# Optimization experiments

Hardware: AMD Instinct MI355X
Metric: run time of the kernel (lower is better)

## Reference

```python
import jax, jax.numpy as jnp
from jax import lax
import numpy as np

IN_F, H1, OUT_F, P = 128, 64, 64, 0.25
B, T = 64, 2048


def setup_inputs() -> dict:
    key = jax.random.key(0)
    ks = jax.random.split(key, 12)
    def w(k, shape, fan_in):
        return jax.random.normal(k, shape, dtype=jnp.float32) / np.sqrt(fan_in).astype(np.float32)
    x = jax.random.normal(ks[0], (B, T, IN_F), dtype=jnp.float32)
    # PyTorch LSTM param layout: W_ih [4H, in], W_hh [4H, H], gate order i,f,g,o
    W_ih1 = w(ks[1], (4 * H1, IN_F), IN_F)
    W_hh1 = w(ks[2], (4 * H1, H1), H1)
    b_ih1 = jnp.zeros((4 * H1,), jnp.float32)
    b_hh1 = jnp.zeros((4 * H1,), jnp.float32)
    W_ih2 = w(ks[3], (4 * OUT_F, H1), H1)
    W_hh2 = w(ks[4], (4 * OUT_F, OUT_F), OUT_F)
    b_ih2 = jnp.zeros((4 * OUT_F,), jnp.float32)
    b_hh2 = jnp.zeros((4 * OUT_F,), jnp.float32)
    # Variational (locked) dropout masks: one per sequence, shared across timesteps,
    # inverted-dropout pre-scaled by 1/(1-p).
    keep = 1.0 - P
    mask1 = (jax.random.bernoulli(ks[5], keep, (B, H1)).astype(jnp.float32) / keep)
    mask2 = (jax.random.bernoulli(ks[6], keep, (B, OUT_F)).astype(jnp.float32) / keep)
    return {"x": x, "W_ih1": W_ih1, "W_hh1": W_hh1, "b_ih1": b_ih1, "b_hh1": b_hh1,
            "W_ih2": W_ih2, "W_hh2": W_hh2, "b_ih2": b_ih2, "b_hh2": b_hh2,
            "mask1": mask1, "mask2": mask2}


def _lstm(x, W_ih, W_hh, b_ih, b_hh):
    # x: [B,T,I]; returns all hidden states [B,T,H]
    Bd = x.shape[0]
    H = W_hh.shape[1]
    # Precompute input contribution for all timesteps (one big GEMM).
    xg = jnp.einsum('bti,gi->btg', x, W_ih) + b_ih + b_hh  # [B,T,4H]
    W_hh_T = W_hh.T  # [H,4H]
    def step(carry, xg_t):
        h, c = carry
        g = xg_t + h @ W_hh_T
        i, f, gg, o = jnp.split(g, 4, axis=-1)
        c = jax.nn.sigmoid(f) * c + jax.nn.sigmoid(i) * jnp.tanh(gg)
        h = jax.nn.sigmoid(o) * jnp.tanh(c)
        return (h, c), h
    h0 = jnp.zeros((Bd, H), x.dtype)
    c0 = jnp.zeros((Bd, H), x.dtype)
    _, hs = lax.scan(step, (h0, c0), jnp.swapaxes(xg, 0, 1))
    return jnp.swapaxes(hs, 0, 1)


def reference(x, W_ih1, W_hh1, b_ih1, b_hh1, W_ih2, W_hh2, b_ih2, b_hh2, mask1, mask2):
    out = _lstm(x, W_ih1, W_hh1, b_ih1, b_hh1) * mask1[:, None, :]
    out = _lstm(out, W_ih2, W_hh2, b_ih2, b_hh2) * mask2[:, None, :]
    return jax.nn.relu(out)
```

## Files before the change

### kernel.cpp

```cpp
#include <hip/hip_runtime.h>
#include <hip/hip_bf16.h>

#define BB 64
#define TT 2048
#define INF 128
#define HH 64
#define GG 256

__device__ __forceinline__ float sigm(float x) { return 1.0f / (1.0f + __expf(-x)); }
__device__ __forceinline__ float tanh_f(float x) {
  float e = __expf(2.0f * x);
  return 1.0f - 2.0f / (e + 1.0f);
}
__device__ __forceinline__ float bcast(float v, int l) {
  return __uint_as_float(__builtin_amdgcn_readlane(__float_as_uint(v), l));
}


#define XWL1(I)                                                   \
  { float4 a = Wp[t * 32 + (I)];                                  \
    w0[4*(I)] = a.x; w0[4*(I)+1] = a.y; w0[4*(I)+2] = a.z; w0[4*(I)+3] = a.w; \
    float4 b = Wp[(128 + t) * 32 + (I)];                          \
    w1[4*(I)] = b.x; w1[4*(I)+1] = b.y; w1[4*(I)+2] = b.z; w1[4*(I)+3] = b.w; }
#define XWL4(I) XWL1(I) XWL1((I)+1) XWL1((I)+2) XWL1((I)+3)
#define XWLOAD XWL4(0) XWL4(4) XWL4(8) XWL4(12) XWL4(16) XWL4(20) XWL4(24) XWL4(28)

#define XD1(L)                                                    \
  { float xa = bcast(curx, (L)); float xb = bcast(cury, (L));     \
    a0e = fmaf(xa, w0[2*(L)],   a0e); a0o = fmaf(xb, w0[2*(L)+1], a0o); \
    a1e = fmaf(xa, w1[2*(L)],   a1e); a1o = fmaf(xb, w1[2*(L)+1], a1o); }
#define XD8(L) XD1(L) XD1((L)+1) XD1((L)+2) XD1((L)+3) XD1((L)+4) XD1((L)+5) XD1((L)+6) XD1((L)+7)
#define XDOT64 XD8(0) XD8(8) XD8(16) XD8(24) XD8(32) XD8(40) XD8(48) XD8(56)

__global__ __launch_bounds__(128, 1) void xgemm(const float* __restrict__ X,
                                                const float* __restrict__ W,
                                                const float* __restrict__ bi,
                                                const float* __restrict__ bh,
                                                float* __restrict__ XG) {
  const int t = threadIdx.x;
  const int lane = t & 63;
  const long m0 = (long)blockIdx.x * 256;

  float w0[INF], w1[INF];
  const float4* Wp = (const float4*)W;
  XWLOAD
  const float bias0 = bi[t] + bh[t];
  const float bias1 = bi[128 + t] + bh[128 + t];

  const float2* Xp = (const float2*)X;
  float2 cur = Xp[(size_t)m0 * 64 + lane];
  float2 nx1 = Xp[(size_t)(m0 + 1) * 64 + lane];

  for (int mi = 0; mi < 256; ++mi) {
    const long m = m0 + mi;
    float2 nx2 = make_float2(0.f, 0.f);
    if (mi + 2 < 256) nx2 = Xp[(size_t)(m + 2) * 64 + lane];

    const float curx = cur.x, cury = cur.y;
    float a0e = bias0, a0o = 0.f, a1e = bias1, a1o = 0.f;
    XDOT64
    XG[(size_t)m * GG + t] = a0e + a0o;
    XG[(size_t)m * GG + 128 + t] = a1e + a1o;
    cur = nx1; nx1 = nx2;
  }
}

#define WL1(I)                                                                  \
  { float4 a = p[lane * 16 + (I)];                                              \
    wi[4*(I)] = a.x; wi[4*(I)+1] = a.y; wi[4*(I)+2] = a.z; wi[4*(I)+3] = a.w;   \
    float4 c = p[(64 + lane) * 16 + (I)];                                       \
    wf[4*(I)] = c.x; wf[4*(I)+1] = c.y; wf[4*(I)+2] = c.z; wf[4*(I)+3] = c.w;   \
    float4 d = p[(128 + lane) * 16 + (I)];                                      \
    wg[4*(I)] = d.x; wg[4*(I)+1] = d.y; wg[4*(I)+2] = d.z; wg[4*(I)+3] = d.w;   \
    float4 e = p[(192 + lane) * 16 + (I)];                                      \
    wo[4*(I)] = e.x; wo[4*(I)+1] = e.y; wo[4*(I)+2] = e.z; wo[4*(I)+3] = e.w; }
#define WL4(I) WL1(I) WL1((I)+1) WL1((I)+2) WL1((I)+3)
#define WLOAD WL4(0) WL4(4) WL4(8) WL4(12)

#define D1(K)                                              \
  { float hk = bcast(hv, (K));                             \
    ai = fmaf(hk, wi[(K)], ai); af = fmaf(hk, wf[(K)], af);\
    ag = fmaf(hk, wg[(K)], ag); ao = fmaf(hk, wo[(K)], ao); }
#define D8(K) D1(K) D1((K)+1) D1((K)+2) D1((K)+3) D1((K)+4) D1((K)+5) D1((K)+6) D1((K)+7)
#define DOT64 D8(0) D8(8) D8(16) D8(24) D8(32) D8(40) D8(48) D8(56)

__global__ __launch_bounds__(256, 1) void lstm2(const float* __restrict__ XG,
                                                const float* __restrict__ Whh1,
                                                const float* __restrict__ Wih2,
                                                const float* __restrict__ Whh2,
                                                const float* __restrict__ bi2,
                                                const float* __restrict__ bh2,
                                                const float* __restrict__ m1g,
                                                const float* __restrict__ m2g,
                                                float* __restrict__ out) {
  const int b = blockIdx.x;
  const int wid = threadIdx.x >> 6;
  const int lane = threadIdx.x & 63;

  __shared__ int f_w0, f_w1, f_w2;
  __shared__ __align__(16) float x2buf[4][HH];
  __shared__ __align__(16) float a2xbuf[4][GG];

  if (threadIdx.x == 0) { f_w0 = 0; f_w1 = 0; f_w2 = 0; }
  __syncthreads();
  if (wid == 3) return;

#define WAIT_GE(flag, tgt)                                   \
  do {                                                       \
    while (*(volatile int*)&(flag) < (tgt)) {}               \
    asm volatile("" ::: "memory");                           \
  } while (0)
#define PUBLISH(flag, val)                                   \
  do {                                                       \
    asm volatile("s_waitcnt lgkmcnt(0)" ::: "memory");       \
    if (lane == 0) *(volatile int*)&(flag) = (val);          \
  } while (0)

  if (wid == 0) {
    float wi[HH], wf[HH], wg[HH], wo[HH];
    const float4* p = (const float4*)Whh1;
    WLOAD
    const float m1 = m1g[b * HH + lane];
    const float* xgp = XG + (size_t)b * TT * GG;

    float cur0 = xgp[lane], cur1 = xgp[64 + lane], cur2 = xgp[128 + lane], cur3 = xgp[192 + lane];
    float n10 = xgp[GG + lane], n11 = xgp[GG + 64 + lane], n12 = xgp[GG + 128 + lane], n13 = xgp[GG + 192 + lane];

    float h1 = 0.f, c1 = 0.f;
    for (int s = 0; s < TT; ++s) {
      float n20 = 0.f, n21 = 0.f, n22 = 0.f, n23 = 0.f;
      if (s + 2 < TT) {
        const float* q = xgp + (size_t)(s + 2) * GG;
        n20 = q[lane]; n21 = q[64 + lane]; n22 = q[128 + lane]; n23 = q[192 + lane];
      }

      const float hv = h1;
      float ai = cur0, af = cur1, ag = cur2, ao = cur3;
      DOT64
      c1 = sigm(af) * c1 + sigm(ai) * tanh_f(ag);
      h1 = sigm(ao) * tanh_f(c1);

      WAIT_GE(f_w1, s - 3);
      x2buf[s & 3][lane] = h1 * m1;
      PUBLISH(f_w0, s + 1);

      cur0 = n10; cur1 = n11; cur2 = n12; cur3 = n13;
      n10 = n20; n11 = n21; n12 = n22; n13 = n23;
    }
  } else if (wid == 1) {
    float wi[HH], wf[HH], wg[HH], wo[HH];
    const float4* p = (const float4*)Wih2;
    WLOAD
    const float bi_i = bi2[lane] + bh2[lane];
    const float bi_f = bi2[64 + lane] + bh2[64 + lane];
    const float bi_g = bi2[128 + lane] + bh2[128 + lane];
    const float bi_o = bi2[192 + lane] + bh2[192 + lane];

    for (int s = 0; s < TT; ++s) {
      WAIT_GE(f_w0, s + 1);
      const float hv = x2buf[s & 3][lane];

      float ai = bi_i, af = bi_f, ag = bi_g, ao = bi_o;
      DOT64
      WAIT_GE(f_w2, s - 3);
      a2xbuf[s & 3][lane] = ai;
      a2xbuf[s & 3][64 + lane] = af;
      a2xbuf[s & 3][128 + lane] = ag;
      a2xbuf[s & 3][192 + lane] = ao;
      PUBLISH(f_w1, s + 1);
    }
  } else {
    float wi[HH], wf[HH], wg[HH], wo[HH];
    const float4* p = (const float4*)Whh2;
    WLOAD
    const float m2 = m2g[b * HH + lane];
    float* ob = out + (size_t)b * TT * HH;

    float h2 = 0.f, c2 = 0.f;
    for (int s = 0; s < TT; ++s) {
      const float hv = h2;
      float ai = 0.f, af = 0.f, ag = 0.f, ao = 0.f;
      DOT64

      WAIT_GE(f_w1, s + 1);
      ai += a2xbuf[s & 3][lane];
      af += a2xbuf[s & 3][64 + lane];
      ag += a2xbuf[s & 3][128 + lane];
      ao += a2xbuf[s & 3][192 + lane];

      c2 = sigm(af) * c2 + sigm(ai) * tanh_f(ag);
      h2 = sigm(ao) * tanh_f(c2);
      PUBLISH(f_w2, s + 1);
      ob[(size_t)s * HH + lane] = fmaxf(h2 * m2, 0.f);
    }
  }
#undef WAIT_GE
#undef PUBLISH
}

extern "C" void kernel_launch(void* const* d_in, const int* in_sizes, int n_in,
                              void* d_out, int out_size, void* d_ws, size_t ws_size,
                              hipStream_t stream) {
  (void)in_sizes; (void)n_in; (void)out_size; (void)ws_size;
  const float* x     = (const float*)d_in[0];
  const float* W_ih1 = (const float*)d_in[1];
  const float* W_hh1 = (const float*)d_in[2];
  const float* b_ih1 = (const float*)d_in[3];
  const float* b_hh1 = (const float*)d_in[4];
  const float* W_ih2 = (const float*)d_in[5];
  const float* W_hh2 = (const float*)d_in[6];
  const float* b_ih2 = (const float*)d_in[7];
  const float* b_hh2 = (const float*)d_in[8];
  const float* mask1 = (const float*)d_in[9];
  const float* mask2 = (const float*)d_in[10];
  float* out = (float*)d_out;

  float* xg1 = (float*)d_ws;

  xgemm<<<dim3(BB * TT / 256), dim3(128), 0, stream>>>(x, W_ih1, b_ih1, b_hh1, xg1);
  lstm2<<<dim3(BB), dim3(256), 0, stream>>>(xg1, W_hh1, W_ih2, W_hh2, b_ih2, b_hh2,
                                            mask1, mask2, out);
}
```

Measured before the change: 2.522 ms.

## Split layer-2 input projection across two waves and deepen LSTM pipeline ring buffers

The previously idle fourth wave now takes the odd timesteps of the layer-2 input projection, so two waves (even/odd) feed the layer-2 recurrence through separate flags. The ring buffers grow from 4 to 8 slots, layer 1 processes two timesteps per publish, flag polls are cached locally to skip redundant LDS reads, and layer 2 speculatively loads its input when it is already available. The xgemm grid also doubles with half the rows per block. The aim is to take the projection wave off the critical path of the serial recurrence, at the cost of more complex synchronization.

Result: slower. 3.867 ms (+53.3%).

```diff
diff --git a/kernel.cpp b/kernel.cpp
--- a/kernel.cpp
+++ b/kernel.cpp
@@ -39,7 +39,7 @@
                                                 float* __restrict__ XG) {
   const int t = threadIdx.x;
   const int lane = t & 63;
-  const long m0 = (long)blockIdx.x * 256;
+  const long m0 = (long)blockIdx.x * 128;
 
   float w0[INF], w1[INF];
   const float4* Wp = (const float4*)W;
@@ -51,10 +51,10 @@
   float2 cur = Xp[(size_t)m0 * 64 + lane];
   float2 nx1 = Xp[(size_t)(m0 + 1) * 64 + lane];
 
-  for (int mi = 0; mi < 256; ++mi) {
+  for (int mi = 0; mi < 128; ++mi) {
     const long m = m0 + mi;
     float2 nx2 = make_float2(0.f, 0.f);
-    if (mi + 2 < 256) nx2 = Xp[(size_t)(m + 2) * 64 + lane];
+    if (mi + 2 < 128) nx2 = Xp[(size_t)(m + 2) * 64 + lane];
 
     const float curx = cur.x, cury = cur.y;
     float a0e = bias0, a0o = 0.f, a1e = bias1, a1o = 0.f;
@@ -97,23 +97,29 @@
   const int wid = threadIdx.x >> 6;
   const int lane = threadIdx.x & 63;
 
-  __shared__ int f_w0, f_w1, f_w2;
-  __shared__ __align__(16) float x2buf[4][HH];
-  __shared__ __align__(16) float a2xbuf[4][GG];
-
-  if (threadIdx.x == 0) { f_w0 = 0; f_w1 = 0; f_w2 = 0; }
+  __shared__ int f_w0, f_e, f_o, f_w2;
+  __shared__ __align__(16) float x2buf[8][HH];
+  __shared__ __align__(16) float a2xbuf[8][GG];
+
+  if (threadIdx.x == 0) { f_w0 = 0; f_e = 0; f_o = 0; f_w2 = 0; }
   __syncthreads();
-  if (wid == 3) return;
-
-#define WAIT_GE(flag, tgt)                                   \
-  do {                                                       \
-    while (*(volatile int*)&(flag) < (tgt)) {}               \
-    asm volatile("" ::: "memory");                           \
+
+#define WAITC(seen, flag, tgt)                                  \
+  do {                                                          \
+    if ((seen) < (tgt)) {                                       \
+      while (((seen) = *(volatile int*)&(flag)) < (tgt)) {}     \
+    }                                                           \
+    asm volatile("" ::: "memory");                              \
   } while (0)
-#define PUBLISH(flag, val)                                   \
-  do {                                                       \
-    asm volatile("s_waitcnt lgkmcnt(0)" ::: "memory");       \
-    if (lane == 0) *(volatile int*)&(flag) = (val);          \
+#define PUBLISH(flag, val)                                      \
+  do {                                                          \
+    asm volatile("s_waitcnt lgkmcnt(0)" ::: "memory");          \
+    if (lane == 0) *(volatile int*)&(flag) = (val);             \
+  } while (0)
+#define PUBLISHP(pflag, val)                                    \
+  do {                                                          \
+    asm volatile("s_waitcnt lgkmcnt(0)" ::: "memory");          \
+    if (lane == 0) *(pflag) = (val);                            \
   } while (0)
 
   if (wid == 0) {
@@ -123,31 +129,87 @@
     const float m1 = m1g[b * HH + lane];
     const float* xgp = XG + (size_t)b * TT * GG;
 
-    float cur0 = xgp[lane], cur1 = xgp[64 + lane], cur2 = xgp[128 + lane], cur3 = xgp[192 + lane];
-    float n10 = xgp[GG + lane], n11 = xgp[GG + 64 + lane], n12 = xgp[GG + 128 + lane], n13 = xgp[GG + 192 + lane];
+    float a0 = xgp[lane], a1 = xgp[64 + lane], a2 = xgp[128 + lane], a3 = xgp[192 + lane];
+    float b0 = xgp[GG + lane], b1 = xgp[GG + 64 + lane], b2 = xgp[GG + 128 + lane], b3 = xgp[GG + 192 + lane];
 
     float h1 = 0.f, c1 = 0.f;
-    for (int s = 0; s < TT; ++s) {
-      float n20 = 0.f, n21 = 0.f, n22 = 0.f, n23 = 0.f;
+    int seen_e = 0, seen_o = 0;
+    for (int s = 0; s < TT; s += 2) {
+      float p0 = 0.f, p1 = 0.f, p2 = 0.f, p3 = 0.f;
+      float q0 = 0.f, q1 = 0.f, q2 = 0.f, q3 = 0.f;
       if (s + 2 < TT) {
         const float* q = xgp + (size_t)(s + 2) * GG;
-        n20 = q[lane]; n21 = q[64 + lane]; n22 = q[128 + lane]; n23 = q[192 + lane];
-      }
-
-      const float hv = h1;
-      float ai = cur0, af = cur1, ag = cur2, ao = cur3;
+        p0 = q[lane]; p1 = q[64 + lane]; p2 = q[128 + lane]; p3 = q[192 + lane];
+        const float* r = q + GG;
+        q0 = r[lane]; q1 = r[64 + lane]; q2 = r[128 + lane]; q3 = r[192 + lane];
+      }
+
+      WAITC(seen_e, f_e, s - 7);
+      WAITC(seen_o, f_o, s - 6);
+
+      {
+        const float hv = h1;
+        float ai = a0, af = a1, ag = a2, ao = a3;
+        DOT64
+        c1 = sigm(af) * c1 + sigm(ai) * tanh_f(ag);
+        h1 = sigm(ao) * tanh_f(c1);
+        x2buf[s & 7][lane] = h1 * m1;
+      }
+      {
+        const float hv = h1;
+        float ai = b0, af = b1, ag = b2, ao = b3;
+        DOT64
+        c1 = sigm(af) * c1 + sigm(ai) * tanh_f(ag);
+        h1 = sigm(ao) * tanh_f(c1);
+        x2buf[(s + 1) & 7][lane] = h1 * m1;
+      }
+      PUBLISH(f_w0, s + 2);
+
+      a0 = p0; a1 = p1; a2 = p2; a3 = p3;
+      b0 = q0; b1 = q1; b2 = q2; b3 = q3;
+    }
+  } else if (wid == 2) {
+    float wi[HH], wf[HH], wg[HH], wo[HH];
+    const float4* p = (const float4*)Whh2;
+    WLOAD
+    const float m2 = m2g[b * HH + lane];
+    float* ob = out + (size_t)b * TT * HH;
+
+    float h2 = 0.f, c2 = 0.f;
+    int seen_e = 0, seen_o = 0;
+    for (int s = 0; s < TT; ++s) {
+      const int odd = s & 1;
+      const bool pre = odd ? (seen_o >= s + 1) : (seen_e >= s + 1);
+      float xi, xf, xg, xo;
+      if (pre) {
+        asm volatile("" ::: "memory");
+        xi = a2xbuf[s & 7][lane];
+        xf = a2xbuf[s & 7][64 + lane];
+        xg = a2xbuf[s & 7][128 + lane];
+        xo = a2xbuf[s & 7][192 + lane];
+      }
+
+      const float hv = h2;
+      float ai = 0.f, af = 0.f, ag = 0.f, ao = 0.f;
       DOT64
-      c1 = sigm(af) * c1 + sigm(ai) * tanh_f(ag);
-      h1 = sigm(ao) * tanh_f(c1);
-
-      WAIT_GE(f_w1, s - 3);
-      x2buf[s & 3][lane] = h1 * m1;
-      PUBLISH(f_w0, s + 1);
-
-      cur0 = n10; cur1 = n11; cur2 = n12; cur3 = n13;
-      n10 = n20; n11 = n21; n12 = n22; n13 = n23;
+
+      if (!pre) {
+        if (odd) { WAITC(seen_o, f_o, s + 1); }
+        else     { WAITC(seen_e, f_e, s + 1); }
+        xi = a2xbuf[s & 7][lane];
+        xf = a2xbuf[s & 7][64 + lane];
+        xg = a2xbuf[s & 7][128 + lane];
+        xo = a2xbuf[s & 7][192 + lane];
+      }
+      ai += xi; af += xf; ag += xg; ao += xo;
+
+      PUBLISH(f_w2, s + 1);
+
+      c2 = sigm(af) * c2 + sigm(ai) * tanh_f(ag);
+      h2 = sigm(ao) * tanh_f(c2);
+      ob[(size_t)s * HH + lane] = fmaxf(h2 * m2, 0.f);
     }
-  } else if (wid == 1) {
+  } else {
     float wi[HH], wf[HH], wg[HH], wo[HH];
     const float4* p = (const float4*)Wih2;
     WLOAD
@@ -156,46 +218,27 @@
     const float bi_g = bi2[128 + lane] + bh2[128 + lane];
     const float bi_o = bi2[192 + lane] + bh2[192 + lane];
 
-    for (int s = 0; s < TT; ++s) {
-      WAIT_GE(f_w0, s + 1);
-      const float hv = x2buf[s & 3][lane];
+    const int par = (wid == 3);
+    volatile int* const myflag = par ? &f_o : &f_e;
+    int seen0 = 0, seen2 = 0;
+    for (int s = par; s < TT; s += 2) {
+      WAITC(seen0, f_w0, s + 1);
+      const float hv = x2buf[s & 7][lane];
 
       float ai = bi_i, af = bi_f, ag = bi_g, ao = bi_o;
       DOT64
-      WAIT_GE(f_w2, s - 3);
-      a2xbuf[s & 3][lane] = ai;
-      a2xbuf[s & 3][64 + lane] = af;
-      a2xbuf[s & 3][128 + lane] = ag;
-      a2xbuf[s & 3][192 + lane] = ao;
-      PUBLISH(f_w1, s + 1);
-    }
-  } else {
-    float wi[HH], wf[HH], wg[HH], wo[HH];
-    const float4* p = (const float4*)Whh2;
-    WLOAD
-    const float m2 = m2g[b * HH + lane];
-    float* ob = out + (size_t)b * TT * HH;
-
-    float h2 = 0.f, c2 = 0.f;
-    for (int s = 0; s < TT; ++s) {
-      const float hv = h2;
-      float ai = 0.f, af = 0.f, ag = 0.f, ao = 0.f;
-      DOT64
-
-      WAIT_GE(f_w1, s + 1);
-      ai += a2xbuf[s & 3][lane];
-      af += a2xbuf[s & 3][64 + lane];
-      ag += a2xbuf[s & 3][128 + lane];
-      ao += a2xbuf[s & 3][192 + lane];
-
-      c2 = sigm(af) * c2 + sigm(ai) * tanh_f(ag);
-      h2 = sigm(ao) * tanh_f(c2);
-      PUBLISH(f_w2, s + 1);
-      ob[(size_t)s * HH + lane] = fmaxf(h2 * m2, 0.f);
+
+      WAITC(seen2, f_w2, s - 7);
+      a2xbuf[s & 7][lane] = ai;
+      a2xbuf[s & 7][64 + lane] = af;
+      a2xbuf[s & 7][128 + lane] = ag;
+      a2xbuf[s & 7][192 + lane] = ao;
+      PUBLISHP(myflag, s + 1);
     }
   }
-#undef WAIT_GE
+#undef WAITC
 #undef PUBLISH
+#undef PUBLISHP
 }
 
 extern "C" void kernel_launch(void* const* d_in, const int* in_sizes, int n_in,
@@ -217,7 +260,7 @@
 
   float* xg1 = (float*)d_ws;
 
-  xgemm<<<dim3(BB * TT / 256), dim3(128), 0, stream>>>(x, W_ih1, b_ih1, b_hh1, xg1);
+  xgemm<<<dim3(BB * TT / 128), dim3(128), 0, stream>>>(x, W_ih1, b_ih1, b_hh1, xg1);
   lstm2<<<dim3(BB), dim3(256), 0, stream>>>(xg1, W_hh1, W_ih2, W_hh2, b_ih2, b_hh2,
                                             mask1, mask2, out);
 }
```

## Split each LSTM recurrence across two wavefronts exchanging gate activations via LDS

Applied to the files above, without the earlier changes.

Each recurrent stage (layer-1 W_hh, layer-2 input projection, layer-2 W_hh) now runs on two wavefronts, each computing two of the four gates. The partner activations are exchanged through double-buffered LDS with flag handshakes, and both halves redundantly keep c and h. This halves the serial per-step FMA chain on the critical path, at the cost of an extra intra-block sync per step. Inter-stage buffers are deepened to 8 slots with cached flag reads, and the xgemm kernel now uses 256 threads with one gate row per thread.

Measured after the change: 2.729 ms. 1.08x slower.

```diff
diff --git a/kernel.cpp b/kernel.cpp
--- a/kernel.cpp
+++ b/kernel.cpp
@@ -15,24 +15,39 @@
 __device__ __forceinline__ float bcast(float v, int l) {
   return __uint_as_float(__builtin_amdgcn_readlane(__float_as_uint(v), l));
 }
-
-
-#define XWL1(I)                                                   \
-  { float4 a = Wp[t * 32 + (I)];                                  \
-    w0[4*(I)] = a.x; w0[4*(I)+1] = a.y; w0[4*(I)+2] = a.z; w0[4*(I)+3] = a.w; \
-    float4 b = Wp[(128 + t) * 32 + (I)];                          \
-    w1[4*(I)] = b.x; w1[4*(I)+1] = b.y; w1[4*(I)+2] = b.z; w1[4*(I)+3] = b.w; }
-#define XWL4(I) XWL1(I) XWL1((I)+1) XWL1((I)+2) XWL1((I)+3)
-#define XWLOAD XWL4(0) XWL4(4) XWL4(8) XWL4(12) XWL4(16) XWL4(20) XWL4(24) XWL4(28)
-
-#define XD1(L)                                                    \
-  { float xa = bcast(curx, (L)); float xb = bcast(cury, (L));     \
-    a0e = fmaf(xa, w0[2*(L)],   a0e); a0o = fmaf(xb, w0[2*(L)+1], a0o); \
-    a1e = fmaf(xa, w1[2*(L)],   a1e); a1o = fmaf(xb, w1[2*(L)+1], a1o); }
-#define XD8(L) XD1(L) XD1((L)+1) XD1((L)+2) XD1((L)+3) XD1((L)+4) XD1((L)+5) XD1((L)+6) XD1((L)+7)
-#define XDOT64 XD8(0) XD8(8) XD8(16) XD8(24) XD8(32) XD8(40) XD8(48) XD8(56)
-
-__global__ __launch_bounds__(128, 1) void xgemm(const float* __restrict__ X,
+__device__ __forceinline__ void lstm_upd(float Si, float Sf, float Tg, float So,
+                                         float& c, float& h) {
+  c = fmaf(Sf, c, Si * Tg);
+  h = So * tanh_f(c);
+}
+
+
+#define WL2(I)                                                                   \
+  { float4 a_ = p[lane * 16 + (I)];                                              \
+    wA[4*(I)] = a_.x; wA[4*(I)+1] = a_.y; wA[4*(I)+2] = a_.z; wA[4*(I)+3] = a_.w;\
+    float4 b_ = p[(64 + lane) * 16 + (I)];                                       \
+    wB[4*(I)] = b_.x; wB[4*(I)+1] = b_.y; wB[4*(I)+2] = b_.z; wB[4*(I)+3] = b_.w; }
+#define WL2x4(I) WL2(I) WL2((I)+1) WL2((I)+2) WL2((I)+3)
+#define WLOAD2 WL2x4(0) WL2x4(4) WL2x4(8) WL2x4(12)
+
+#define G1(K)                                                    \
+  { float hk = bcast(hv, (K));                                   \
+    aA = fmaf(hk, wA[(K)], aA); aB = fmaf(hk, wB[(K)], aB); }
+#define G8(K) G1(K) G1((K)+1) G1((K)+2) G1((K)+3) G1((K)+4) G1((K)+5) G1((K)+6) G1((K)+7)
+#define DOT2G G8(0) G8(8) G8(16) G8(24) G8(32) G8(40) G8(48) G8(56)
+
+#define YW1(I) { float4 a_ = Wp[t * 32 + (I)];                                   \
+    wr[4*(I)] = a_.x; wr[4*(I)+1] = a_.y; wr[4*(I)+2] = a_.z; wr[4*(I)+3] = a_.w; }
+#define YW4(I) YW1(I) YW1((I)+1) YW1((I)+2) YW1((I)+3)
+#define YWLOAD YW4(0) YW4(4) YW4(8) YW4(12) YW4(16) YW4(20) YW4(24) YW4(28)
+
+#define YD1(L)                                                   \
+  { float xa = bcast(curx, (L)); float xb = bcast(cury, (L));    \
+    ae = fmaf(xa, wr[2*(L)], ae); ao = fmaf(xb, wr[2*(L)+1], ao); }
+#define YD8(L) YD1(L) YD1((L)+1) YD1((L)+2) YD1((L)+3) YD1((L)+4) YD1((L)+5) YD1((L)+6) YD1((L)+7)
+#define YDOT64 YD8(0) YD8(8) YD8(16) YD8(24) YD8(32) YD8(40) YD8(48) YD8(56)
+
+__global__ __launch_bounds__(256, 1) void xgemm(const float* __restrict__ X,
                                                 const float* __restrict__ W,
                                                 const float* __restrict__ bi,
                                                 const float* __restrict__ bh,
@@ -41,11 +56,10 @@
   const int lane = t & 63;
   const long m0 = (long)blockIdx.x * 256;
 
-  float w0[INF], w1[INF];
+  float wr[INF];
   const float4* Wp = (const float4*)W;
-  XWLOAD
-  const float bias0 = bi[t] + bh[t];
-  const float bias1 = bi[128 + t] + bh[128 + t];
+  YWLOAD
+  const float bias = bi[t] + bh[t];
 
   const float2* Xp = (const float2*)X;
   float2 cur = Xp[(size_t)m0 * 64 + lane];
@@ -57,34 +71,14 @@
     if (mi + 2 < 256) nx2 = Xp[(size_t)(m + 2) * 64 + lane];
 
     const float curx = cur.x, cury = cur.y;
-    float a0e = bias0, a0o = 0.f, a1e = bias1, a1o = 0.f;
-    XDOT64
-    XG[(size_t)m * GG + t] = a0e + a0o;
-    XG[(size_t)m * GG + 128 + t] = a1e + a1o;
+    float ae = bias, ao = 0.f;
+    YDOT64
+    XG[(size_t)m * GG + t] = ae + ao;
     cur = nx1; nx1 = nx2;
   }
 }
 
-#define WL1(I)                                                                  \
-  { float4 a = p[lane * 16 + (I)];                                              \
-    wi[4*(I)] = a.x; wi[4*(I)+1] = a.y; wi[4*(I)+2] = a.z; wi[4*(I)+3] = a.w;   \
-    float4 c = p[(64 + lane) * 16 + (I)];                                       \
-    wf[4*(I)] = c.x; wf[4*(I)+1] = c.y; wf[4*(I)+2] = c.z; wf[4*(I)+3] = c.w;   \
-    float4 d = p[(128 + lane) * 16 + (I)];                                      \
-    wg[4*(I)] = d.x; wg[4*(I)+1] = d.y; wg[4*(I)+2] = d.z; wg[4*(I)+3] = d.w;   \
-    float4 e = p[(192 + lane) * 16 + (I)];                                      \
-    wo[4*(I)] = e.x; wo[4*(I)+1] = e.y; wo[4*(I)+2] = e.z; wo[4*(I)+3] = e.w; }
-#define WL4(I) WL1(I) WL1((I)+1) WL1((I)+2) WL1((I)+3)
-#define WLOAD WL4(0) WL4(4) WL4(8) WL4(12)
-
-#define D1(K)                                              \
-  { float hk = bcast(hv, (K));                             \
-    ai = fmaf(hk, wi[(K)], ai); af = fmaf(hk, wf[(K)], af);\
-    ag = fmaf(hk, wg[(K)], ag); ao = fmaf(hk, wo[(K)], ao); }
-#define D8(K) D1(K) D1((K)+1) D1((K)+2) D1((K)+3) D1((K)+4) D1((K)+5) D1((K)+6) D1((K)+7)
-#define DOT64 D8(0) D8(8) D8(16) D8(24) D8(32) D8(40) D8(48) D8(56)
-
-__global__ __launch_bounds__(256, 1) void lstm2(const float* __restrict__ XG,
+__global__ __launch_bounds__(384, 1) void lstm2(const float* __restrict__ XG,
                                                 const float* __restrict__ Whh1,
                                                 const float* __restrict__ Wih2,
                                                 const float* __restrict__ Whh2,
@@ -97,104 +91,173 @@
   const int wid = threadIdx.x >> 6;
   const int lane = threadIdx.x & 63;
 
-  __shared__ int f_w0, f_w1, f_w2;
-  __shared__ __align__(16) float x2buf[4][HH];
-  __shared__ __align__(16) float a2xbuf[4][GG];
-
-  if (threadIdx.x == 0) { f_w0 = 0; f_w1 = 0; f_w2 = 0; }
+  __shared__ int f_0A, f_0B, f_h1, f_xA, f_xB, f_2A, f_2B;
+  __shared__ __align__(16) float ex0A[2][2 * HH];
+  __shared__ __align__(16) float ex0B[2][2 * HH];
+  __shared__ __align__(16) float ex2A[2][2 * HH];
+  __shared__ __align__(16) float ex2B[2][2 * HH];
+  __shared__ __align__(16) float x2buf[8][HH];
+  __shared__ __align__(16) float a2xA[8][2 * HH];
+  __shared__ __align__(16) float a2xB[8][2 * HH];
+
+  if (threadIdx.x == 0) { f_0A = 0; f_0B = 0; f_h1 = 0; f_xA = 0; f_xB = 0; f_2A = 0; f_2B = 0; }
   __syncthreads();
-  if (wid == 3) return;
-
-#define WAIT_GE(flag, tgt)                                   \
-  do {                                                       \
-    while (*(volatile int*)&(flag) < (tgt)) {}               \
-    asm volatile("" ::: "memory");                           \
+
+#define WAITC(seen, flag, tgt)                                  \
+  do {                                                          \
+    if ((seen) < (tgt)) {                                       \
+      while (((seen) = *(volatile int*)&(flag)) < (tgt)) {}     \
+    }                                                           \
+    asm volatile("" ::: "memory");                              \
   } while (0)
-#define PUBLISH(flag, val)                                   \
-  do {                                                       \
-    asm volatile("s_waitcnt lgkmcnt(0)" ::: "memory");       \
-    if (lane == 0) *(volatile int*)&(flag) = (val);          \
+#define PUBLISH(flag, val)                                      \
+  do {                                                          \
+    asm volatile("s_waitcnt lgkmcnt(0)" ::: "memory");          \
+    if (lane == 0) *(volatile int*)&(flag) = (val);             \
   } while (0)
 
-  if (wid == 0) {
-    float wi[HH], wf[HH], wg[HH], wo[HH];
+  if (wid == 2) {
+    float wA[HH], wB[HH];
     const float4* p = (const float4*)Whh1;
-    WLOAD
+    WLOAD2
     const float m1 = m1g[b * HH + lane];
     const float* xgp = XG + (size_t)b * TT * GG;
 
-    float cur0 = xgp[lane], cur1 = xgp[64 + lane], cur2 = xgp[128 + lane], cur3 = xgp[192 + lane];
-    float n10 = xgp[GG + lane], n11 = xgp[GG + 64 + lane], n12 = xgp[GG + 128 + lane], n13 = xgp[GG + 192 + lane];
+    float xi0 = xgp[lane],      xf0 = xgp[64 + lane];
+    float xi1 = xgp[GG + lane], xf1 = xgp[GG + 64 + lane];
 
     float h1 = 0.f, c1 = 0.f;
-    for (int s = 0; s < TT; ++s) {
-      float n20 = 0.f, n21 = 0.f, n22 = 0.f, n23 = 0.f;
+    int s0B = 0, sxa = 0, sxb = 0;
+    for (int s = 0; s < TT; ++s) {
+      float xi2 = 0.f, xf2 = 0.f;
       if (s + 2 < TT) {
         const float* q = xgp + (size_t)(s + 2) * GG;
-        n20 = q[lane]; n21 = q[64 + lane]; n22 = q[128 + lane]; n23 = q[192 + lane];
+        xi2 = q[lane]; xf2 = q[64 + lane];
       }
-
       const float hv = h1;
-      float ai = cur0, af = cur1, ag = cur2, ao = cur3;
-      DOT64
-      c1 = sigm(af) * c1 + sigm(ai) * tanh_f(ag);
-      h1 = sigm(ao) * tanh_f(c1);
-
-      WAIT_GE(f_w1, s - 3);
-      x2buf[s & 3][lane] = h1 * m1;
-      PUBLISH(f_w0, s + 1);
-
-      cur0 = n10; cur1 = n11; cur2 = n12; cur3 = n13;
-      n10 = n20; n11 = n21; n12 = n22; n13 = n23;
-    }
-  } else if (wid == 1) {
-    float wi[HH], wf[HH], wg[HH], wo[HH];
+      float aA = xi0, aB = xf0;
+      DOT2G
+      const float Si = sigm(aA), Sf = sigm(aB);
+      ex0A[s & 1][lane] = Si; ex0A[s & 1][64 + lane] = Sf;
+      PUBLISH(f_0A, s + 1);
+      WAITC(s0B, f_0B, s + 1);
+      const float Tg = ex0B[s & 1][lane], So = ex0B[s & 1][64 + lane];
+      lstm_upd(Si, Sf, Tg, So, c1, h1);
+      WAITC(sxa, f_xA, s - 7);
+      WAITC(sxb, f_xB, s - 7);
+      x2buf[s & 7][lane] = h1 * m1;
+      PUBLISH(f_h1, s + 1);
+      xi0 = xi1; xf0 = xf1; xi1 = xi2; xf1 = xf2;
+    }
+  } else if (wid == 0) {
+    float wA[HH], wB[HH];
+    const float4* p = (const float4*)(Whh1 + 128 * HH);
+    WLOAD2
+    const float* xgp = XG + (size_t)b * TT * GG;
+
+    float xg0 = xgp[128 + lane],      xo0 = xgp[192 + lane];
+    float xg1 = xgp[GG + 128 + lane], xo1 = xgp[GG + 192 + lane];
+
+    float h1 = 0.f, c1 = 0.f;
+    int s0A = 0;
+    for (int s = 0; s < TT; ++s) {
+      float xg2 = 0.f, xo2 = 0.f;
+      if (s + 2 < TT) {
+        const float* q = xgp + (size_t)(s + 2) * GG;
+        xg2 = q[128 + lane]; xo2 = q[192 + lane];
+      }
+      const float hv = h1;
+      float aA = xg0, aB = xo0;
+      DOT2G
+      const float Tg = tanh_f(aA), So = sigm(aB);
+      ex0B[s & 1][lane] = Tg; ex0B[s & 1][64 + lane] = So;
+      PUBLISH(f_0B, s + 1);
+      WAITC(s0A, f_0A, s + 1);
+      const float Si = ex0A[s & 1][lane], Sf = ex0A[s & 1][64 + lane];
+      lstm_upd(Si, Sf, Tg, So, c1, h1);
+      xg0 = xg1; xo0 = xo1; xg1 = xg2; xo1 = xo2;
+    }
+  } else if (wid == 4) {
+    float wA[HH], wB[HH];
     const float4* p = (const float4*)Wih2;
-    WLOAD
-    const float bi_i = bi2[lane] + bh2[lane];
-    const float bi_f = bi2[64 + lane] + bh2[64 + lane];
-    const float bi_g = bi2[128 + lane] + bh2[128 + lane];
-    const float bi_o = bi2[192 + lane] + bh2[192 + lane];
-
-    for (int s = 0; s < TT; ++s) {
-      WAIT_GE(f_w0, s + 1);
-      const float hv = x2buf[s & 3][lane];
-
-      float ai = bi_i, af = bi_f, ag = bi_g, ao = bi_o;
-      DOT64
-      WAIT_GE(f_w2, s - 3);
-      a2xbuf[s & 3][lane] = ai;
-      a2xbuf[s & 3][64 + lane] = af;
-      a2xbuf[s & 3][128 + lane] = ag;
-      a2xbuf[s & 3][192 + lane] = ao;
-      PUBLISH(f_w1, s + 1);
+    WLOAD2
+    const float biA = bi2[lane] + bh2[lane];
+    const float biB = bi2[64 + lane] + bh2[64 + lane];
+
+    int sh = 0, sc = 0;
+    for (int s = 0; s < TT; ++s) {
+      WAITC(sh, f_h1, s + 1);
+      const float hv = x2buf[s & 7][lane];
+      float aA = biA, aB = biB;
+      DOT2G
+      WAITC(sc, f_2A, s - 7);
+      a2xA[s & 7][lane] = aA; a2xA[s & 7][64 + lane] = aB;
+      PUBLISH(f_xA, s + 1);
+    }
+  } else if (wid == 5) {
+    float wA[HH], wB[HH];
+    const float4* p = (const float4*)(Wih2 + 128 * HH);
+    WLOAD2
+    const float biA = bi2[128 + lane] + bh2[128 + lane];
+    const float biB = bi2[192 + lane] + bh2[192 + lane];
+
+    int sh = 0, sc = 0;
+    for (int s = 0; s < TT; ++s) {
+      WAITC(sh, f_h1, s + 1);
+      const float hv = x2buf[s & 7][lane];
+      float aA = biA, aB = biB;
+      DOT2G
+      WAITC(sc, f_2B, s - 7);
+      a2xB[s & 7][lane] = aA; a2xB[s & 7][64 + lane] = aB;
+      PUBLISH(f_xB, s + 1);
+    }
+  } else if (wid == 3) {
+    float wA[HH], wB[HH];
+    const float4* p = (const float4*)Whh2;
+    WLOAD2
+    const float m2v = m2g[b * HH + lane];
+    float* ob = out + (size_t)b * TT * HH;
+
+    float h2 = 0.f, c2 = 0.f;
+    int sx = 0, s2B = 0;
+    for (int s = 0; s < TT; ++s) {
+      WAITC(sx, f_xA, s + 1);
+      const float pi = a2xA[s & 7][lane], pf = a2xA[s & 7][64 + lane];
+      const float hv = h2;
+      float aA = 0.f, aB = 0.f;
+      DOT2G
+      aA += pi; aB += pf;
+      const float Si = sigm(aA), Sf = sigm(aB);
+      ex2A[s & 1][lane] = Si; ex2A[s & 1][64 + lane] = Sf;
+      PUBLISH(f_2A, s + 1);
+      WAITC(s2B, f_2B, s + 1);
+      const float Tg = ex2B[s & 1][lane], So = ex2B[s & 1][64 + lane];
+      lstm_upd(Si, Sf, Tg, So, c2, h2);
+      ob[(size_t)s * HH + lane] = fmaxf(h2 * m2v, 0.f);
     }
   } else {
-    float wi[HH], wf[HH], wg[HH], wo[HH];
-    const float4* p = (const float4*)Whh2;
-    WLOAD
-    const float m2 = m2g[b * HH + lane];
-    float* ob = out + (size_t)b * TT * HH;
+    float wA[HH], wB[HH];
+    const float4* p = (const float4*)(Whh2 + 128 * HH);
+    WLOAD2
 
     float h2 = 0.f, c2 = 0.f;
-    for (int s = 0; s < TT; ++s) {
+    int sx = 0, s2A = 0;
+    for (int s = 0; s < TT; ++s) {
+      WAITC(sx, f_xB, s + 1);
+      const float pg = a2xB[s & 7][lane], po = a2xB[s & 7][64 + lane];
       const float hv = h2;
-      float ai = 0.f, af = 0.f, ag = 0.f, ao = 0.f;
-      DOT64
-
-      WAIT_GE(f_w1, s + 1);
-      ai += a2xbuf[s & 3][lane];
-      af += a2xbuf[s & 3][64 + lane];
-      ag += a2xbuf[s & 3][128 + lane];
-      ao += a2xbuf[s & 3][192 + lane];
-
-      c2 = sigm(af) * c2 + sigm(ai) * tanh_f(ag);
-      h2 = sigm(ao) * tanh_f(c2);
-      PUBLISH(f_w2, s + 1);
-      ob[(size_t)s * HH + lane] = fmaxf(h2 * m2, 0.f);
+      float aA = 0.f, aB = 0.f;
+      DOT2G
+      aA += pg; aB += po;
+      const float Tg = tanh_f(aA), So = sigm(aB);
+      ex2B[s & 1][lane] = Tg; ex2B[s & 1][64 + lane] = So;
+      PUBLISH(f_2B, s + 1);
+      WAITC(s2A, f_2A, s + 1);
+      const float Si = ex2A[s & 1][lane], Sf = ex2A[s & 1][64 + lane];
+      lstm_upd(Si, Sf, Tg, So, c2, h2);
     }
   }
-#undef WAIT_GE
+#undef WAITC
 #undef PUBLISH
 }
 
@@ -217,7 +280,7 @@
 
   float* xg1 = (float*)d_ws;
 
-  xgemm<<<dim3(BB * TT / 256), dim3(128), 0, stream>>>(x, W_ih1, b_ih1, b_hh1, xg1);
-  lstm2<<<dim3(BB), dim3(256), 0, stream>>>(xg1, W_hh1, W_ih2, W_hh2, b_ih2, b_hh2,
+  xgemm<<<dim3(BB * TT / 256), dim3(256), 0, stream>>>(x, W_ih1, b_ih1, b_hh1, xg1);
+  lstm2<<<dim3(BB), dim3(384), 0, stream>>>(xg1, W_hh1, W_ih2, W_hh2, b_ih2, b_hh2,
                                             mask1, mask2, out);
 }
```

## Split layer-2 input projection across two waves and deepen ring buffers

Applied to the files above, without the earlier changes.

The per-sequence LSTM kernel now uses its idle fourth wave. The layer-2 input projection is split over two waves that handle even and odd timesteps, each with its own flag, and the ring buffers grow from 4 to 8 slots. Spin-waits cache the last seen flag value to skip redundant LDS polls. The xgemm kernel now runs 256 threads, each computing one gate column, which halves register weight storage per thread. Together these aim to take the middle pipeline stage off the critical path, at the cost of more synchronization complexity.

Measured after the change: 2.442 ms. 3.1% less time.

```diff
diff --git a/kernel.cpp b/kernel.cpp
--- a/kernel.cpp
+++ b/kernel.cpp
@@ -16,54 +16,6 @@
   return __uint_as_float(__builtin_amdgcn_readlane(__float_as_uint(v), l));
 }
 
-
-#define XWL1(I)                                                   \
-  { float4 a = Wp[t * 32 + (I)];                                  \
-    w0[4*(I)] = a.x; w0[4*(I)+1] = a.y; w0[4*(I)+2] = a.z; w0[4*(I)+3] = a.w; \
-    float4 b = Wp[(128 + t) * 32 + (I)];                          \
-    w1[4*(I)] = b.x; w1[4*(I)+1] = b.y; w1[4*(I)+2] = b.z; w1[4*(I)+3] = b.w; }
-#define XWL4(I) XWL1(I) XWL1((I)+1) XWL1((I)+2) XWL1((I)+3)
-#define XWLOAD XWL4(0) XWL4(4) XWL4(8) XWL4(12) XWL4(16) XWL4(20) XWL4(24) XWL4(28)
-
-#define XD1(L)                                                    \
-  { float xa = bcast(curx, (L)); float xb = bcast(cury, (L));     \
-    a0e = fmaf(xa, w0[2*(L)],   a0e); a0o = fmaf(xb, w0[2*(L)+1], a0o); \
-    a1e = fmaf(xa, w1[2*(L)],   a1e); a1o = fmaf(xb, w1[2*(L)+1], a1o); }
-#define XD8(L) XD1(L) XD1((L)+1) XD1((L)+2) XD1((L)+3) XD1((L)+4) XD1((L)+5) XD1((L)+6) XD1((L)+7)
-#define XDOT64 XD8(0) XD8(8) XD8(16) XD8(24) XD8(32) XD8(40) XD8(48) XD8(56)
-
-__global__ __launch_bounds__(128, 1) void xgemm(const float* __restrict__ X,
-                                                const float* __restrict__ W,
-                                                const float* __restrict__ bi,
-                                                const float* __restrict__ bh,
-                                                float* __restrict__ XG) {
-  const int t = threadIdx.x;
-  const int lane = t & 63;
-  const long m0 = (long)blockIdx.x * 256;
-
-  float w0[INF], w1[INF];
-  const float4* Wp = (const float4*)W;
-  XWLOAD
-  const float bias0 = bi[t] + bh[t];
-  const float bias1 = bi[128 + t] + bh[128 + t];
-
-  const float2* Xp = (const float2*)X;
-  float2 cur = Xp[(size_t)m0 * 64 + lane];
-  float2 nx1 = Xp[(size_t)(m0 + 1) * 64 + lane];
-
-  for (int mi = 0; mi < 256; ++mi) {
-    const long m = m0 + mi;
-    float2 nx2 = make_float2(0.f, 0.f);
-    if (mi + 2 < 256) nx2 = Xp[(size_t)(m + 2) * 64 + lane];
-
-    const float curx = cur.x, cury = cur.y;
-    float a0e = bias0, a0o = 0.f, a1e = bias1, a1o = 0.f;
-    XDOT64
-    XG[(size_t)m * GG + t] = a0e + a0o;
-    XG[(size_t)m * GG + 128 + t] = a1e + a1o;
-    cur = nx1; nx1 = nx2;
-  }
-}
 
 #define WL1(I)                                                                  \
   { float4 a = p[lane * 16 + (I)];                                              \
@@ -84,36 +36,81 @@
 #define D8(K) D1(K) D1((K)+1) D1((K)+2) D1((K)+3) D1((K)+4) D1((K)+5) D1((K)+6) D1((K)+7)
 #define DOT64 D8(0) D8(8) D8(16) D8(24) D8(32) D8(40) D8(48) D8(56)
 
-__global__ __launch_bounds__(256, 1) void lstm2(const float* __restrict__ XG,
-                                                const float* __restrict__ Whh1,
-                                                const float* __restrict__ Wih2,
-                                                const float* __restrict__ Whh2,
-                                                const float* __restrict__ bi2,
-                                                const float* __restrict__ bh2,
-                                                const float* __restrict__ m1g,
-                                                const float* __restrict__ m2g,
-                                                float* __restrict__ out) {
+#define YW1(I) { float4 a_ = Wp[t * 32 + (I)];                                   \
+    wr[4*(I)] = a_.x; wr[4*(I)+1] = a_.y; wr[4*(I)+2] = a_.z; wr[4*(I)+3] = a_.w; }
+#define YW4(I) YW1(I) YW1((I)+1) YW1((I)+2) YW1((I)+3)
+#define YWLOAD YW4(0) YW4(4) YW4(8) YW4(12) YW4(16) YW4(20) YW4(24) YW4(28)
+
+#define YD1(L)                                                   \
+  { float xa = bcast(curx, (L)); float xb = bcast(cury, (L));    \
+    ae = fmaf(xa, wr[2*(L)], ae); ao = fmaf(xb, wr[2*(L)+1], ao); }
+#define YD8(L) YD1(L) YD1((L)+1) YD1((L)+2) YD1((L)+3) YD1((L)+4) YD1((L)+5) YD1((L)+6) YD1((L)+7)
+#define YDOT64 YD8(0) YD8(8) YD8(16) YD8(24) YD8(32) YD8(40) YD8(48) YD8(56)
+
+__global__ __launch_bounds__(256, 1) void xgemm(const float* __restrict__ X,
+                                                const float* __restrict__ W,
+                                                const float* __restrict__ bi,
+                                                const float* __restrict__ bh,
+                                                float* __restrict__ XG) {
+  const int t = threadIdx.x;
+  const int lane = t & 63;
+  const long m0 = (long)blockIdx.x * 256;
+
+  float wr[INF];
+  const float4* Wp = (const float4*)W;
+  YWLOAD
+  const float bias = bi[t] + bh[t];
+
+  const float2* Xp = (const float2*)X;
+  float2 cur = Xp[(size_t)m0 * 64 + lane];
+  float2 nx1 = Xp[(size_t)(m0 + 1) * 64 + lane];
+
+  for (int mi = 0; mi < 256; ++mi) {
+    const long m = m0 + mi;
+    float2 nx2 = make_float2(0.f, 0.f);
+    if (mi + 2 < 256) nx2 = Xp[(size_t)(m + 2) * 64 + lane];
+
+    const float curx = cur.x, cury = cur.y;
+    float ae = bias, ao = 0.f;
+    YDOT64
+    XG[(size_t)m * GG + t] = ae + ao;
+    cur = nx1; nx1 = nx2;
+  }
+}
+
+__global__ __attribute__((amdgpu_flat_work_group_size(256, 256),
+                          amdgpu_waves_per_eu(1, 1)))
+void lstm2(const float* __restrict__ XG,
+           const float* __restrict__ Whh1,
+           const float* __restrict__ Wih2,
+           const float* __restrict__ Whh2,
+           const float* __restrict__ bi2,
+           const float* __restrict__ bh2,
+           const float* __restrict__ m1g,
+           const float* __restrict__ m2g,
+           float* __restrict__ out) {
   const int b = blockIdx.x;
   const int wid = threadIdx.x >> 6;
   const int lane = threadIdx.x & 63;
 
-  __shared__ int f_w0, f_w1, f_w2;
-  __shared__ __align__(16) float x2buf[4][HH];
-  __shared__ __align__(16) float a2xbuf[4][GG];
-
-  if (threadIdx.x == 0) { f_w0 = 0; f_w1 = 0; f_w2 = 0; }
+  __shared__ int f_h1, f_xe, f_xo, f_2;
+  __shared__ __align__(16) float x2buf[8][HH];
+  __shared__ __align__(16) float a2xbuf[8][GG];
+
+  if (threadIdx.x == 0) { f_h1 = 0; f_xe = 0; f_xo = 0; f_2 = 0; }
   __syncthreads();
-  if (wid == 3) return;
-
-#define WAIT_GE(flag, tgt)                                   \
-  do {                                                       \
-    while (*(volatile int*)&(flag) < (tgt)) {}               \
-    asm volatile("" ::: "memory");                           \
+
+#define WAITC(seen, flag, tgt)                                  \
+  do {                                                          \
+    if ((seen) < (tgt)) {                                       \
+      while (((seen) = *(volatile int*)&(flag)) < (tgt)) {}     \
+    }                                                           \
+    asm volatile("" ::: "memory");                              \
   } while (0)
-#define PUBLISH(flag, val)                                   \
-  do {                                                       \
-    asm volatile("s_waitcnt lgkmcnt(0)" ::: "memory");       \
-    if (lane == 0) *(volatile int*)&(flag) = (val);          \
+#define PUBLISH(flag, val)                                      \
+  do {                                                          \
+    asm volatile("s_waitcnt lgkmcnt(0)" ::: "memory");          \
+    if (lane == 0) *(volatile int*)&(flag) = (val);             \
   } while (0)
 
   if (wid == 0) {
@@ -127,6 +124,7 @@
     float n10 = xgp[GG + lane], n11 = xgp[GG + 64 + lane], n12 = xgp[GG + 128 + lane], n13 = xgp[GG + 192 + lane];
 
     float h1 = 0.f, c1 = 0.f;
+    int sxe = 0, sxo = 0;
     for (int s = 0; s < TT; ++s) {
       float n20 = 0.f, n21 = 0.f, n22 = 0.f, n23 = 0.f;
       if (s + 2 < TT) {
@@ -140,14 +138,42 @@
       c1 = sigm(af) * c1 + sigm(ai) * tanh_f(ag);
       h1 = sigm(ao) * tanh_f(c1);
 
-      WAIT_GE(f_w1, s - 3);
-      x2buf[s & 3][lane] = h1 * m1;
-      PUBLISH(f_w0, s + 1);
+      if (s & 1) { WAITC(sxo, f_xo, s - 7); }
+      else       { WAITC(sxe, f_xe, s - 7); }
+      x2buf[s & 7][lane] = h1 * m1;
+      PUBLISH(f_h1, s + 1);
 
       cur0 = n10; cur1 = n11; cur2 = n12; cur3 = n13;
       n10 = n20; n11 = n21; n12 = n22; n13 = n23;
     }
-  } else if (wid == 1) {
+  } else if (wid == 3) {
+    float wi[HH], wf[HH], wg[HH], wo[HH];
+    const float4* p = (const float4*)Whh2;
+    WLOAD
+    const float m2v = m2g[b * HH + lane];
+    float* ob = out + (size_t)b * TT * HH;
+
+    float h2 = 0.f, c2 = 0.f;
+    int sxe = 0, sxo = 0;
+    for (int s = 0; s < TT; ++s) {
+      if (s & 1) { WAITC(sxo, f_xo, s + 1); }
+      else       { WAITC(sxe, f_xe, s + 1); }
+      const float pi = a2xbuf[s & 7][lane];
+      const float pf = a2xbuf[s & 7][64 + lane];
+      const float pg = a2xbuf[s & 7][128 + lane];
+      const float po = a2xbuf[s & 7][192 + lane];
+
+      const float hv = h2;
+      float ai = 0.f, af = 0.f, ag = 0.f, ao = 0.f;
+      DOT64
+      ai += pi; af += pf; ag += pg; ao += po;
+
+      c2 = sigm(af) * c2 + sigm(ai) * tanh_f(ag);
+      h2 = sigm(ao) * tanh_f(c2);
+      PUBLISH(f_2, s + 1);
+      ob[(size_t)s * HH + lane] = fmaxf(h2 * m2v, 0.f);
+    }
+  } else {
     float wi[HH], wf[HH], wg[HH], wo[HH];
     const float4* p = (const float4*)Wih2;
     WLOAD
@@ -156,45 +182,25 @@
     const float bi_g = bi2[128 + lane] + bh2[128 + lane];
     const float bi_o = bi2[192 + lane] + bh2[192 + lane];
 
-    for (int s = 0; s < TT; ++s) {
-      WAIT_GE(f_w0, s + 1);
-      const float hv = x2buf[s & 3][lane];
+    const int par = wid - 1;
+    volatile int* const myflag = par ? (volatile int*)&f_xo : (volatile int*)&f_xe;
+    int s0 = 0, s2 = 0;
+    for (int s = par; s < TT; s += 2) {
+      WAITC(s0, f_h1, s + 1);
+      const float hv = x2buf[s & 7][lane];
 
       float ai = bi_i, af = bi_f, ag = bi_g, ao = bi_o;
       DOT64
-      WAIT_GE(f_w2, s - 3);
-      a2xbuf[s & 3][lane] = ai;
-      a2xbuf[s & 3][64 + lane] = af;
-      a2xbuf[s & 3][128 + lane] = ag;
-      a2xbuf[s & 3][192 + lane] = ao;
-      PUBLISH(f_w1, s + 1);
-    }
-  } else {
-    float wi[HH], wf[HH], wg[HH], wo[HH];
-    const float4* p = (const float4*)Whh2;
-    WLOAD
-    const float m2 = m2g[b * HH + lane];
-    float* ob = out + (size_t)b * TT * HH;
-
-    float h2 = 0.f, c2 = 0.f;
-    for (int s = 0; s < TT; ++s) {
-      const float hv = h2;
-      float ai = 0.f, af = 0.f, ag = 0.f, ao = 0.f;
-      DOT64
-
-      WAIT_GE(f_w1, s + 1);
-      ai += a2xbuf[s & 3][lane];
-      af += a2xbuf[s & 3][64 + lane];
-      ag += a2xbuf[s & 3][128 + lane];
-      ao += a2xbuf[s & 3][192 + lane];
-
-      c2 = sigm(af) * c2 + sigm(ai) * tanh_f(ag);
-      h2 = sigm(ao) * tanh_f(c2);
-      PUBLISH(f_w2, s + 1);
-      ob[(size_t)s * HH + lane] = fmaxf(h2 * m2, 0.f);
+
+      WAITC(s2, f_2, s - 7);
+      a2xbuf[s & 7][lane] = ai;
+      a2xbuf[s & 7][64 + lane] = af;
+      a2xbuf[s & 7][128 + lane] = ag;
+      a2xbuf[s & 7][192 + lane] = ao;
+      PUBLISH(*myflag, s + 1);
     }
   }
-#undef WAIT_GE
+#undef WAITC
 #undef PUBLISH
 }
 
@@ -217,7 +223,7 @@
 
   float* xg1 = (float*)d_ws;
 
-  xgemm<<<dim3(BB * TT / 256), dim3(128), 0, stream>>>(x, W_ih1, b_ih1, b_hh1, xg1);
+  xgemm<<<dim3(BB * TT / 256), dim3(256), 0, stream>>>(x, W_ih1, b_ih1, b_hh1, xg1);
   lstm2<<<dim3(BB), dim3(256), 0, stream>>>(xg1, W_hh1, W_ih2, W_hh2, b_ih2, b_hh2,
                                             mask1, mask2, out);
 }
```
